# Kernel optimization log

Hardware: AMD Instinct MI355X
Metric: run time of the kernel (lower is better)

Reference implementation:

```python
import jax, jax.numpy as jnp
import numpy as np

D_IN = 1024
D_EMB = 512
HIDDEN = 256
NUM_CLASSES = 64
N_SUPPORT = 4096
N_QUERY = 8192


def setup_inputs() -> dict:
    key = jax.random.key(0)
    ks = jax.random.split(key, 8)
    scale_e = 1.0 / np.sqrt(D_IN)
    scale_1 = 1.0 / np.sqrt(2 * D_EMB)
    scale_2 = 1.0 / np.sqrt(HIDDEN)
    return {
        "support_data": jax.random.normal(ks[0], (N_SUPPORT, D_IN), jnp.float32),
        "query_data": jax.random.normal(ks[1], (N_QUERY, D_IN), jnp.float32),
        "support_label": jax.random.randint(ks[2], (N_SUPPORT,), 0, NUM_CLASSES, jnp.int32),
        "W_e": jax.random.normal(ks[3], (D_IN, D_EMB), jnp.float32) * scale_e,
        "b_e": jnp.zeros((D_EMB,), jnp.float32),
        "W1": jax.random.normal(ks[4], (2 * D_EMB, HIDDEN), jnp.float32) * scale_1,
        "b1": jnp.zeros((HIDDEN,), jnp.float32),
        "W2": jax.random.normal(ks[5], (HIDDEN, 1), jnp.float32) * scale_2,
        "b2": jnp.zeros((1,), jnp.float32),
    }


def reference(support_data, query_data, support_label, W_e, b_e, W1, b1, W2, b2):
    # embedding_net: Linear + ReLU
    s_emb = jax.nn.relu(support_data @ W_e + b_e)  # [Ns, D_EMB]
    q_emb = jax.nn.relu(query_data @ W_e + b_e)    # [Nq, D_EMB]

    # per-class mean of support embeddings (segment mean; labels are 0..C-1,
    # matching torch.unique()'s sorted order)
    sums = jax.ops.segment_sum(s_emb, support_label, num_segments=NUM_CLASSES)
    counts = jax.ops.segment_sum(jnp.ones((s_emb.shape[0],), s_emb.dtype),
                                 support_label, num_segments=NUM_CLASSES)
    means = sums / jnp.maximum(counts, 1.0)[:, None]  # [C, D_EMB]

    # relation_net on concat(query, class_mean): split first linear so the
    # [Nq*C, 2*D_EMB] concat is never materialized (same math).
    Wq, Wc = W1[:D_EMB], W1[D_EMB:]
    h = jax.nn.relu(q_emb @ Wq[:, None, :].squeeze(1) @ jnp.eye(HIDDEN, dtype=W1.dtype)
                    if False else
                    (q_emb @ Wq)[:, None, :] + (means @ Wc)[None, :, :] + b1)  # [Nq, C, HIDDEN]
    scores = jax.nn.sigmoid(h @ W2 + b2)  # [Nq, C, 1]
    # torch version stacks [1,1]-shaped scores -> [Nq, C, 1, 1]
    return scores[:, :, None, :]
```

## Files before the change

kernel.cpp:

```cpp
#include <hip/hip_runtime.h>
#include <hip/hip_bf16.h>

#define D_IN 1024
#define D_EMB 512
#define HIDDEN 256
#define NUM_CLASSES 64
#define N_SUPPORT 4096
#define N_QUERY 8192

typedef __bf16 bf16x8 __attribute__((ext_vector_type(8)));
typedef __bf16 bf16x4 __attribute__((ext_vector_type(4)));
typedef float f32x4 __attribute__((ext_vector_type(4)));

#define GLOAD_LDS16(g, l)                                                          \
  __builtin_amdgcn_global_load_lds(                                                \
      (const __attribute__((address_space(1))) unsigned int*)(g),                  \
      (__attribute__((address_space(3))) unsigned int*)(l), 16, 0, 0)

__global__ __launch_bounds__(256) void prep(
    const float* __restrict__ W_e, const float* __restrict__ W1,
    const float* __restrict__ support, const float* __restrict__ query,
    __bf16* __restrict__ WeT, __bf16* __restrict__ WqT,
    __bf16* __restrict__ Xbf) {
  const int tid = threadIdx.x;
  int b = blockIdx.x;
  if (b < 640) {
    __shared__ float tile[32][33];
    const float* in;
    __bf16* out;
    int bx, by, rows, cols;
    if (b < 512) {
      in = W_e; out = WeT; rows = D_IN; cols = D_EMB;
      bx = (b & 15) * 32; by = (b >> 4) * 32;
    } else {
      b -= 512;
      in = W1; out = WqT; rows = D_EMB; cols = HIDDEN;
      bx = (b & 7) * 32; by = (b >> 3) * 32;
    }
    int tx = tid & 31, ty = tid >> 5;
#pragma unroll
    for (int i = ty; i < 32; i += 8)
      tile[i][tx] = in[(long)(by + i) * cols + bx + tx];
    __syncthreads();
#pragma unroll
    for (int i = ty; i < 32; i += 8)
      out[(long)(bx + i) * rows + by + tx] = (__bf16)tile[tx][i];
  } else {
    const long nsup = (long)N_SUPPORT * D_IN;
    long base = (long)(b - 640) * 4096;
#pragma unroll
    for (int g = 0; g < 4; ++g) {
      long i = base + g * 1024 + tid * 4;
      const float* src = (i < nsup) ? (support + i) : (query + (i - nsup));
      float4 v = *(const float4*)src;
      bf16x4 o;
      o[0] = (__bf16)v.x; o[1] = (__bf16)v.y;
      o[2] = (__bf16)v.z; o[3] = (__bf16)v.w;
      *(bf16x4*)(Xbf + i) = o;
    }
  }
}

template <int BM, int BN, int K, bool OUT_BF16>
__global__ __launch_bounds__(256, 4) void gemm_pipe(
    const __bf16* __restrict__ A, const __bf16* __restrict__ BT,
    const float* __restrict__ bias, void* __restrict__ Cv, int Ncols) {
  constexpr int BK = 32;
  constexpr int NT = K / BK;
  constexpr int MR = BM / 32;
  constexpr int NR = BN / 32;
  constexpr int AQ = BM * 4 / 256;
  constexpr int LOADS = AQ + 1;

  __shared__ __align__(16) __bf16 As[3][BM * BK];
  __shared__ __align__(16) __bf16 Bs[3][BN * BK];

  const int tid = threadIdx.x;
  const int wave = tid >> 6, lane = tid & 63;
  const int wr = wave >> 1, wc = wave & 1;
  const int l16 = lane & 15, half = lane >> 4;
  const int slot = half ^ ((l16 >> 1) & 3);

  const int m0 = blockIdx.x * BM;
  const int n0 = blockIdx.y * BN;

  f32x4 acc[MR][NR];
#pragma unroll
  for (int m = 0; m < MR; ++m)
#pragma unroll
    for (int n = 0; n < NR; ++n) acc[m][n] = (f32x4)0.0f;

#define STAGE(t, buf)                                                       \
  {                                                                         \
    _Pragma("unroll") for (int q = 0; q < AQ; ++q) {                        \
      int chunk = q * 256 + tid;                                            \
      int row = chunk >> 2;                                                 \
      int kc = (chunk & 3) ^ ((row >> 1) & 3);                              \
      GLOAD_LDS16(A + (long)(m0 + row) * K + (t) * BK + kc * 8,             \
                  &As[buf][chunk * 8]);                                     \
    }                                                                       \
    {                                                                       \
      int chunk = tid;                                                      \
      int row = chunk >> 2;                                                 \
      int kc = (chunk & 3) ^ ((row >> 1) & 3);                              \
      GLOAD_LDS16(BT + (long)(n0 + row) * K + (t) * BK + kc * 8,            \
                  &Bs[buf][chunk * 8]);                                     \
    }                                                                       \
  }

#define COMPUTE(buf)                                                        \
  {                                                                         \
    bf16x8 a[MR], b[NR];                                                    \
    _Pragma("unroll") for (int m = 0; m < MR; ++m)                          \
        a[m] = *(const bf16x8*)(&As[buf][(wr * (BM / 2) + m * 16 + l16) *   \
                                             BK + slot * 8]);               \
    _Pragma("unroll") for (int n = 0; n < NR; ++n)                          \
        b[n] = *(const bf16x8*)(&Bs[buf][(wc * (BN / 2) + n * 16 + l16) *   \
                                             BK + slot * 8]);               \
    asm volatile("s_waitcnt lgkmcnt(0)" ::: "memory");                      \
    __builtin_amdgcn_sched_barrier(0);                                      \
    _Pragma("unroll") for (int m = 0; m < MR; ++m)                          \
        _Pragma("unroll") for (int n = 0; n < NR; ++n)                      \
            acc[m][n] = __builtin_amdgcn_mfma_f32_16x16x32_bf16(            \
                a[m], b[n], acc[m][n], 0, 0, 0);                            \
  }

#define WAIT_PREV()                                                         \
  if constexpr (LOADS == 3) {                                               \
    asm volatile("s_waitcnt vmcnt(3)" ::: "memory");                        \
  } else {                                                                  \
    asm volatile("s_waitcnt vmcnt(2)" ::: "memory");                        \
  }

  STAGE(0, 0);
  STAGE(1, 1);
  WAIT_PREV();
  __builtin_amdgcn_s_barrier();

  int cur = 0;
  for (int t = 0; t < NT - 2; ++t) {
    int nb = cur + 2;
    if (nb >= 3) nb -= 3;
    STAGE(t + 2, nb);
    COMPUTE(cur);
    WAIT_PREV();
    __builtin_amdgcn_s_barrier();
    cur = (cur + 1 == 3) ? 0 : cur + 1;
  }
  COMPUTE(cur);
  asm volatile("s_waitcnt vmcnt(0)" ::: "memory");
  __builtin_amdgcn_s_barrier();
  cur = (cur + 1 == 3) ? 0 : cur + 1;
  COMPUTE(cur);

#undef STAGE
#undef COMPUTE
#undef WAIT_PREV

#pragma unroll
  for (int m = 0; m < MR; ++m)
#pragma unroll
    for (int n = 0; n < NR; ++n) {
      const int col = n0 + wc * (BN / 2) + n * 16 + l16;
      const float bv = bias[col];
#pragma unroll
      for (int j = 0; j < 4; ++j) {
        int row = m0 + wr * (BM / 2) + m * 16 + half * 4 + j;
        float v = acc[m][n][j] + bv;
        if (OUT_BF16) {
          v = fmaxf(v, 0.0f);
          ((__bf16*)Cv)[(long)row * Ncols + col] = (__bf16)v;
        } else {
          ((float*)Cv)[(long)row * Ncols + col] = v;
        }
      }
    }
}

__global__ __launch_bounds__(256) void proto_partial(
    const __bf16* __restrict__ s_emb, const int* __restrict__ labels,
    float* __restrict__ sums_part, int* __restrict__ cnt_part) {
  const int c = blockIdx.x;
  const int s = blockIdx.y;
  const int tid = threadIdx.x;
  const int j0 = s * (N_SUPPORT / 8);
  float a0 = 0.0f, a1 = 0.0f;
  int count = 0;
#pragma unroll 4
  for (int j = j0; j < j0 + N_SUPPORT / 8; j += 4) {
    int4 lab4 = *(const int4*)(labels + j);
#pragma unroll
    for (int u = 0; u < 4; ++u) {
      int lab = (u == 0) ? lab4.x : (u == 1) ? lab4.y : (u == 2) ? lab4.z : lab4.w;
      if (lab == c) {
        const __bf16* r = s_emb + (long)(j + u) * D_EMB;
        a0 += (float)r[tid];
        a1 += (float)r[tid + 256];
        ++count;
      }
    }
  }
  float* dst = sums_part + (long)(c * 8 + s) * D_EMB;
  dst[tid] = a0;
  dst[tid + 256] = a1;
  if (tid == 0) cnt_part[c * 8 + s] = count;
}

__global__ __launch_bounds__(256) void proto_cpb(
    const float* __restrict__ sums_part, const int* __restrict__ cnt_part,
    const float* __restrict__ W1, float* __restrict__ cpb_part) {
  __shared__ float ls[128];
  const int c = blockIdx.x;
  const int kc = blockIdx.y;
  const int k0 = kc * 128;
  const int tid = threadIdx.x;

  int nc = 0;
#pragma unroll
  for (int s = 0; s < 8; ++s) nc += cnt_part[c * 8 + s];
  float inv = 1.0f / fmaxf((float)nc, 1.0f);

  if (tid < 128) {
    float v = 0.0f;
#pragma unroll
    for (int s = 0; s < 8; ++s)
      v += sums_part[(long)(c * 8 + s) * D_EMB + k0 + tid];
    ls[tid] = v * inv;
  }
  __syncthreads();

  float acc = 0.0f;
#pragma unroll 8
  for (int k = 0; k < 128; ++k)
    acc = fmaf(ls[k], W1[(long)(D_EMB + k0 + k) * HIDDEN + tid], acc);
  cpb_part[((long)kc * NUM_CLASSES + c) * HIDDEN + tid] = acc;
}

__global__ __launch_bounds__(256) void score_kernel(
    const float* __restrict__ qp, const float* __restrict__ cpb_part,
    const float* __restrict__ W2, const float* __restrict__ b2,
    float* __restrict__ out) {
  constexpr int CPB_S = 260;
  __shared__ __align__(16) float cpb_s[NUM_CLASSES * CPB_S];
  __shared__ __align__(16) float qp_s[32 * HIDDEN];
  __shared__ __align__(16) float w2_s[HIDDEN];

  const int tid = threadIdx.x;
  const int w = tid >> 6;
  const int c = tid & 63;
  const int qb0 = blockIdx.x * 32;
  constexpr int NCH = NUM_CLASSES * HIDDEN;

  w2_s[tid] = W2[tid];
  for (int i = tid; i < NCH; i += 256)
    cpb_s[(i >> 8) * CPB_S + (i & (HIDDEN - 1))] =
        cpb_part[i] + cpb_part[NCH + i] + cpb_part[2 * NCH + i] +
        cpb_part[3 * NCH + i];
  for (int i = tid; i < 32 * HIDDEN; i += 256)
    qp_s[i] = qp[(long)qb0 * HIDDEN + i];
  __syncthreads();

  const float bb = b2[0];
  float acc[8];
#pragma unroll
  for (int q = 0; q < 8; ++q) acc[q] = 0.0f;

  const float* crow = cpb_s + c * CPB_S;
  const float* qbase = qp_s + (w * 8) * HIDDEN;

#pragma unroll 4
  for (int kc = 0; kc < HIDDEN / 4; ++kc) {
    f32x4 cv = *(const f32x4*)(crow + kc * 4);
    f32x4 wv = *(const f32x4*)(w2_s + kc * 4);
#pragma unroll
    for (int q = 0; q < 8; ++q) {
      f32x4 qv = *(const f32x4*)(qbase + q * HIDDEN + kc * 4);
      acc[q] = fmaf(fmaxf(qv[0] + cv[0], 0.0f), wv[0], acc[q]);
      acc[q] = fmaf(fmaxf(qv[1] + cv[1], 0.0f), wv[1], acc[q]);
      acc[q] = fmaf(fmaxf(qv[2] + cv[2], 0.0f), wv[2], acc[q]);
      acc[q] = fmaf(fmaxf(qv[3] + cv[3], 0.0f), wv[3], acc[q]);
    }
  }

#pragma unroll
  for (int q = 0; q < 8; ++q) {
    float x = acc[q] + bb;
    out[(long)(qb0 + w * 8 + q) * NUM_CLASSES + c] = 1.0f / (1.0f + __expf(-x));
  }
}

extern "C" void kernel_launch(void* const* d_in, const int* in_sizes, int n_in,
                              void* d_out, int out_size, void* d_ws,
                              size_t ws_size, hipStream_t stream) {
  const float* support = (const float*)d_in[0];
  const float* query   = (const float*)d_in[1];
  const int*   labels  = (const int*)d_in[2];
  const float* W_e     = (const float*)d_in[3];
  const float* b_e     = (const float*)d_in[4];
  const float* W1      = (const float*)d_in[5];
  const float* b1      = (const float*)d_in[6];
  const float* W2      = (const float*)d_in[7];
  const float* b2      = (const float*)d_in[8];
  float* out = (float*)d_out;

  char* ws = (char*)d_ws;
  size_t off = 0;
  auto alloc = [&](size_t bytes) {
    void* p = ws + off;
    off = (off + bytes + 255) & ~(size_t)255;
    return p;
  };
  const long NTOT = N_SUPPORT + N_QUERY;
  __bf16* Xbf = (__bf16*)alloc((size_t)NTOT * D_IN * 2);
  __bf16* WeT = (__bf16*)alloc((size_t)D_EMB * D_IN * 2);
  __bf16* WqT = (__bf16*)alloc((size_t)HIDDEN * D_EMB * 2);
  __bf16* emb = (__bf16*)alloc((size_t)NTOT * D_EMB * 2);
  float*  qp  = (float*)alloc((size_t)N_QUERY * HIDDEN * 4);
  float*  sums_part = (float*)alloc((size_t)NUM_CLASSES * 8 * D_EMB * 4);
  int*    cnt_part  = (int*)alloc((size_t)NUM_CLASSES * 8 * 4);
  float*  cpb_part  = (float*)alloc((size_t)4 * NUM_CLASSES * HIDDEN * 4);

  prep<<<640 + (int)(NTOT * D_IN / 4096), 256, 0, stream>>>(
      W_e, W1, support, query, WeT, WqT, Xbf);

  gemm_pipe<128, 64, D_IN, true>
      <<<dim3(NTOT / 128, D_EMB / 64), 256, 0, stream>>>(
          Xbf, WeT, b_e, emb, D_EMB);

  proto_partial<<<dim3(NUM_CLASSES, 8), 256, 0, stream>>>(emb, labels, sums_part,
                                                          cnt_part);
  proto_cpb<<<dim3(NUM_CLASSES, 4), 256, 0, stream>>>(sums_part, cnt_part, W1,
                                                      cpb_part);

  gemm_pipe<64, 64, D_EMB, false>
      <<<dim3(N_QUERY / 64, HIDDEN / 64), 256, 0, stream>>>(
          emb + (long)N_SUPPORT * D_EMB, WqT, b1, qp, HIDDEN);

  score_kernel<<<N_QUERY / 32, 256, 0, stream>>>(qp, cpb_part, W2, b2, out);
}
```

Measured before the change: 97.25 us.

## Fuse fp32-to-bf16 input conversion into embedding GEMM A-tile loads

The embedding GEMM now reads the fp32 support and query rows directly. It loads them into registers with inline global_load_dwordx4, converts them to bf16, and writes swizzled tiles into LDS. This removes the separate conversion pass and the bf16 copy of X in the workspace, saving one large write and a large read of global memory. In exchange, every N-block re-reads the fp32 inputs at twice the bytes, and the pipeline drops from triple-buffered global-to-LDS loads to a double-buffered register-staged path with explicit waits.

```diff
diff --git a/kernel.cpp b/kernel.cpp
--- a/kernel.cpp
+++ b/kernel.cpp
@@ -17,48 +17,162 @@
       (const __attribute__((address_space(1))) unsigned int*)(g),                  \
       (__attribute__((address_space(3))) unsigned int*)(l), 16, 0, 0)
 
+#define GLOBAL_LOAD_F4(dst, ptr, off)                                              \
+  asm volatile("global_load_dwordx4 %0, %1, off offset:" #off                      \
+               : "=v"(dst) : "v"(ptr) : "memory")
+
 __global__ __launch_bounds__(256) void prep(
     const float* __restrict__ W_e, const float* __restrict__ W1,
+    __bf16* __restrict__ WeT, __bf16* __restrict__ WqT) {
+  __shared__ float tile[32][33];
+  const int tid = threadIdx.x;
+  int b = blockIdx.x;
+  const float* in;
+  __bf16* out;
+  int bx, by, rows, cols;
+  if (b < 512) {
+    in = W_e; out = WeT; rows = D_IN; cols = D_EMB;
+    bx = (b & 15) * 32; by = (b >> 4) * 32;
+  } else {
+    b -= 512;
+    in = W1; out = WqT; rows = D_EMB; cols = HIDDEN;
+    bx = (b & 7) * 32; by = (b >> 3) * 32;
+  }
+  int tx = tid & 31, ty = tid >> 5;
+#pragma unroll
+  for (int i = ty; i < 32; i += 8)
+    tile[i][tx] = in[(long)(by + i) * cols + bx + tx];
+  __syncthreads();
+#pragma unroll
+  for (int i = ty; i < 32; i += 8)
+    out[(long)(bx + i) * rows + by + tx] = (__bf16)tile[tx][i];
+}
+
+__global__ __launch_bounds__(256, 4) void gemm_embf(
     const float* __restrict__ support, const float* __restrict__ query,
-    __bf16* __restrict__ WeT, __bf16* __restrict__ WqT,
-    __bf16* __restrict__ Xbf) {
-  const int tid = threadIdx.x;
-  int b = blockIdx.x;
-  if (b < 640) {
-    __shared__ float tile[32][33];
-    const float* in;
-    __bf16* out;
-    int bx, by, rows, cols;
-    if (b < 512) {
-      in = W_e; out = WeT; rows = D_IN; cols = D_EMB;
-      bx = (b & 15) * 32; by = (b >> 4) * 32;
-    } else {
-      b -= 512;
-      in = W1; out = WqT; rows = D_EMB; cols = HIDDEN;
-      bx = (b & 7) * 32; by = (b >> 3) * 32;
+    const __bf16* __restrict__ BT, const float* __restrict__ bias,
+    __bf16* __restrict__ C) {
+  constexpr int BM = 128, BN = 64, BK = 32;
+  constexpr int N = D_EMB, K = D_IN;
+  constexpr int NT = K / BK;
+  constexpr int MR = 4, NR = 2;
+
+  __shared__ __align__(16) __bf16 As[2][BM * BK];
+  __shared__ __align__(16) __bf16 Bs[2][BN * BK];
+
+  const int tid = threadIdx.x;
+  const int wave = tid >> 6, lane = tid & 63;
+  const int wr = wave >> 1, wc = wave & 1;
+  const int l16 = lane & 15, half = lane >> 4;
+  const int slot = half ^ ((l16 >> 1) & 3);
+
+  const int m0 = blockIdx.x * BM;
+  const int n0 = blockIdx.y * BN;
+
+  const float* Abase = (m0 < N_SUPPORT)
+                           ? support + (long)m0 * K
+                           : query + (long)(m0 - N_SUPPORT) * K;
+
+  const int arow = tid >> 1;
+  const int ach = tid & 1;
+  const float* aptr = Abase + (long)arow * K + ach * 16;
+  const int asw = (arow >> 1) & 3;
+  const int aoff0 = arow * BK + ((ach * 2) ^ asw) * 8;
+  const int aoff1 = arow * BK + ((ach * 2 + 1) ^ asw) * 8;
+
+  const int brow = tid >> 2;
+  const int bkc = (tid & 3) ^ ((brow >> 1) & 3);
+  const __bf16* bptr = BT + (long)(n0 + brow) * K + bkc * 8;
+
+  float4 av0, av1, av2, av3;
+
+  f32x4 acc[MR][NR];
+#pragma unroll
+  for (int m = 0; m < MR; ++m)
+#pragma unroll
+    for (int n = 0; n < NR; ++n) acc[m][n] = (f32x4)0.0f;
+
+#define LOAD_A(t)                                                           \
+  {                                                                         \
+    const float* p = aptr + (t) * BK;                                       \
+    GLOBAL_LOAD_F4(av0, p, 0);                                              \
+    GLOBAL_LOAD_F4(av1, p, 16);                                             \
+    GLOBAL_LOAD_F4(av2, p, 32);                                             \
+    GLOBAL_LOAD_F4(av3, p, 48);                                             \
+  }
+
+#define GLD_B(t, buf) GLOAD_LDS16(bptr + (t) * BK, &Bs[buf][tid * 8])
+
+#define CVT_WRITE(buf)                                                      \
+  {                                                                         \
+    asm volatile("s_waitcnt vmcnt(1)" ::: "memory");                        \
+    __builtin_amdgcn_sched_barrier(0);                                      \
+    bf16x8 o0, o1;                                                          \
+    o0[0] = (__bf16)av0.x; o0[1] = (__bf16)av0.y;                           \
+    o0[2] = (__bf16)av0.z; o0[3] = (__bf16)av0.w;                           \
+    o0[4] = (__bf16)av1.x; o0[5] = (__bf16)av1.y;                           \
+    o0[6] = (__bf16)av1.z; o0[7] = (__bf16)av1.w;                           \
+    o1[0] = (__bf16)av2.x; o1[1] = (__bf16)av2.y;                           \
+    o1[2] = (__bf16)av2.z; o1[3] = (__bf16)av2.w;                           \
+    o1[4] = (__bf16)av3.x; o1[5] = (__bf16)av3.y;                           \
+    o1[6] = (__bf16)av3.z; o1[7] = (__bf16)av3.w;                           \
+    *(bf16x8*)(&As[buf][aoff0]) = o0;                                       \
+    *(bf16x8*)(&As[buf][aoff1]) = o1;                                       \
+  }
+
+#define COMPUTE(buf)                                                        \
+  {                                                                         \
+    bf16x8 a[MR], b[NR];                                                    \
+    _Pragma("unroll") for (int m = 0; m < MR; ++m)                          \
+        a[m] = *(const bf16x8*)(&As[buf][(wr * 64 + m * 16 + l16) * BK +    \
+                                         slot * 8]);                        \
+    _Pragma("unroll") for (int n = 0; n < NR; ++n)                          \
+        b[n] = *(const bf16x8*)(&Bs[buf][(wc * 32 + n * 16 + l16) * BK +    \
+                                         slot * 8]);                        \
+    asm volatile("s_waitcnt lgkmcnt(0)" ::: "memory");                      \
+    __builtin_amdgcn_sched_barrier(0);                                      \
+    _Pragma("unroll") for (int m = 0; m < MR; ++m)                          \
+        _Pragma("unroll") for (int n = 0; n < NR; ++n)                      \
+            acc[m][n] = __builtin_amdgcn_mfma_f32_16x16x32_bf16(            \
+                a[m], b[n], acc[m][n], 0, 0, 0);                            \
+  }
+
+  LOAD_A(0);
+  GLD_B(0, 0);
+  CVT_WRITE(0);
+  asm volatile("s_waitcnt vmcnt(0) lgkmcnt(0)" ::: "memory");
+  __builtin_amdgcn_s_barrier();
+
+  int cur = 0;
+  for (int t = 0; t < NT - 1; ++t) {
+    LOAD_A(t + 1);
+    GLD_B(t + 1, cur ^ 1);
+    COMPUTE(cur);
+    CVT_WRITE(cur ^ 1);
+    asm volatile("s_waitcnt vmcnt(0) lgkmcnt(0)" ::: "memory");
+    __builtin_amdgcn_s_barrier();
+    cur ^= 1;
+  }
+  COMPUTE(cur);
+
+#undef LOAD_A
+#undef GLD_B
+#undef CVT_WRITE
+#undef COMPUTE
+
+#pragma unroll
+  for (int m = 0; m < MR; ++m)
+#pragma unroll
+    for (int n = 0; n < NR; ++n) {
+      const int col = n0 + wc * 32 + n * 16 + l16;
+      const float bv = bias[col];
+#pragma unroll
+      for (int j = 0; j < 4; ++j) {
+        int row = m0 + wr * 64 + m * 16 + half * 4 + j;
+        float v = fmaxf(acc[m][n][j] + bv, 0.0f);
+        C[(long)row * N + col] = (__bf16)v;
+      }
     }
-    int tx = tid & 31, ty = tid >> 5;
-#pragma unroll
-    for (int i = ty; i < 32; i += 8)
-      tile[i][tx] = in[(long)(by + i) * cols + bx + tx];
-    __syncthreads();
-#pragma unroll
-    for (int i = ty; i < 32; i += 8)
-      out[(long)(bx + i) * rows + by + tx] = (__bf16)tile[tx][i];
-  } else {
-    const long nsup = (long)N_SUPPORT * D_IN;
-    long base = (long)(b - 640) * 4096;
-#pragma unroll
-    for (int g = 0; g < 4; ++g) {
-      long i = base + g * 1024 + tid * 4;
-      const float* src = (i < nsup) ? (support + i) : (query + (i - nsup));
-      float4 v = *(const float4*)src;
-      bf16x4 o;
-      o[0] = (__bf16)v.x; o[1] = (__bf16)v.y;
-      o[2] = (__bf16)v.z; o[3] = (__bf16)v.w;
-      *(bf16x4*)(Xbf + i) = o;
-    }
-  }
 }
 
 template <int BM, int BN, int K, bool OUT_BF16>
@@ -311,7 +425,6 @@
     return p;
   };
   const long NTOT = N_SUPPORT + N_QUERY;
-  __bf16* Xbf = (__bf16*)alloc((size_t)NTOT * D_IN * 2);
   __bf16* WeT = (__bf16*)alloc((size_t)D_EMB * D_IN * 2);
   __bf16* WqT = (__bf16*)alloc((size_t)HIDDEN * D_EMB * 2);
   __bf16* emb = (__bf16*)alloc((size_t)NTOT * D_EMB * 2);
@@ -320,12 +433,10 @@
   int*    cnt_part  = (int*)alloc((size_t)NUM_CLASSES * 8 * 4);
   float*  cpb_part  = (float*)alloc((size_t)4 * NUM_CLASSES * HIDDEN * 4);
 
-  prep<<<640 + (int)(NTOT * D_IN / 4096), 256, 0, stream>>>(
-      W_e, W1, support, query, WeT, WqT, Xbf);
-
-  gemm_pipe<128, 64, D_IN, true>
-      <<<dim3(NTOT / 128, D_EMB / 64), 256, 0, stream>>>(
-          Xbf, WeT, b_e, emb, D_EMB);
+  prep<<<640, 256, 0, stream>>>(W_e, W1, WeT, WqT);
+
+  gemm_embf<<<dim3(NTOT / 128, D_EMB / 64), 256, 0, stream>>>(
+      support, query, WeT, b_e, emb);
 
   proto_partial<<<dim3(NUM_CLASSES, 8), 256, 0, stream>>>(emb, labels, sums_part,
                                                           cnt_part);
```

New measurement: 107.0 us. 10.0% more time.
